# Optimization experiments

Hardware: AMD Instinct MI355X
Metric: run time of the kernel (lower is better)

Reference implementation:

```python
import jax, jax.numpy as jnp
import numpy as np
from jax import lax

# mamba-130m-style config
B, L = 2, 1024          # batch, seq_len
D = 768                 # hidden_size
E = 1536                # intermediate (expand=2)
N = 16                  # ssm state size
R = 48                  # time_step_rank = ceil(D/16)
K = 4                   # conv kernel
NL = 4                  # num layers
NC = 5                  # num classes
EPS = 1e-5


def setup_inputs() -> dict:
    key = jax.random.key(0)
    ks = jax.random.split(key, 10)
    s = 0.02
    return {
        "x": jax.random.normal(ks[0], (B, L, 12), dtype=jnp.float32),
        "proj_w": jax.random.normal(ks[1], (D, 12)) * s,
        "proj_b": jnp.zeros((D,), jnp.float32),
        "norm_w": jnp.ones((NL, D), jnp.float32),
        "in_w": jax.random.normal(ks[2], (NL, 2 * E, D)) * s,
        "conv_w": jax.random.normal(ks[3], (NL, E, K)) * s,
        "conv_b": jnp.zeros((NL, E), jnp.float32),
        "xproj_w": jax.random.normal(ks[4], (NL, R + 2 * N, E)) * s,
        "dt_w": jax.random.normal(ks[5], (NL, E, R)) * s,
        "dt_b": jnp.full((NL, E), -4.0, jnp.float32),  # softplus(-4) ~ small dt
        "A_log": jnp.tile(jnp.log(jnp.arange(1, N + 1, dtype=jnp.float32))[None, None, :], (NL, E, 1)),
        "D_param": jnp.ones((NL, E), jnp.float32),
        "out_w": jax.random.normal(ks[6], (NL, D, E)) * s,
        "fnorm_w": jnp.ones((D,), jnp.float32),
        "cls_w": jax.random.normal(ks[7], (NC, D)) * s,
        "cls_b": jnp.zeros((NC,), jnp.float32),
    }


def _rmsnorm(x, w):
    var = jnp.mean(x * x, axis=-1, keepdims=True)
    return x * lax.rsqrt(var + EPS) * w


def _causal_conv(u, w, b):
    # u: [B,L,E], w: [E,K] depthwise causal conv, left-pad K-1
    up = jnp.pad(u, ((0, 0), (K - 1, 0), (0, 0)))
    y = b
    for k in range(K):
        y = y + w[:, k] * up[:, k:k + L, :]
    return y


def _selective_scan(u, dt, A, Bm, Cm, Dp):
    # u, dt: [B,L,E]; Bm, Cm: [B,L,N]; A: [E,N]; Dp: [E]
    def step(h, inp):
        u_t, dt_t, B_t, C_t = inp  # [B,E],[B,E],[B,N],[B,N]
        dA = jnp.exp(dt_t[:, :, None] * A)                      # [B,E,N]
        h = h * dA + dt_t[:, :, None] * B_t[:, None, :] * u_t[:, :, None]
        y = jnp.einsum('ben,bn->be', h, C_t)
        return h, y

    h0 = jnp.zeros((u.shape[0], E, N), u.dtype)
    _, ys = lax.scan(step, h0,
                     (u.transpose(1, 0, 2), dt.transpose(1, 0, 2),
                      Bm.transpose(1, 0, 2), Cm.transpose(1, 0, 2)))
    return ys.transpose(1, 0, 2) + u * Dp


def reference(x, proj_w, proj_b, norm_w, in_w, conv_w, conv_b, xproj_w,
              dt_w, dt_b, A_log, D_param, out_w, fnorm_w, cls_w, cls_b):
    h = x @ proj_w.T + proj_b                                     # [B,L,D]
    for i in range(NL):
        res = h
        hn = _rmsnorm(h, norm_w[i])
        proj = hn @ in_w[i].T                                     # [B,L,2E]
        u, gate = proj[..., :E], proj[..., E:]
        u = jax.nn.silu(_causal_conv(u, conv_w[i], conv_b[i]))    # [B,L,E]
        xdbc = u @ xproj_w[i].T                                   # [B,L,R+2N]
        dt_r = xdbc[..., :R]
        Bm = xdbc[..., R:R + N]
        Cm = xdbc[..., R + N:]
        dt = jax.nn.softplus(dt_r @ dt_w[i].T + dt_b[i])          # [B,L,E]
        A = -jnp.exp(A_log[i])                                    # [E,N]
        y = _selective_scan(u, dt, A, Bm, Cm, D_param[i])
        y = y * jax.nn.silu(gate)
        h = res + y @ out_w[i].T
    h = _rmsnorm(h, fnorm_w)
    pooled = jnp.mean(h, axis=1)                                  # AdaptiveAvgPool1d(1)
    return pooled @ cls_w.T + cls_b                               # [B,NC]
```

## Files before the change

kernel.cpp:

```cpp
#include <hip/hip_runtime.h>

constexpr int B_  = 2;
constexpr int L_  = 1024;
constexpr int D_  = 768;
constexpr int E_  = 1536;
constexpr int N_  = 16;
constexpr int R_  = 48;
constexpr int NL_ = 4;
constexpr int NC_ = 5;
constexpr int M_  = B_ * L_;
constexpr int E2_ = 2 * E_;
constexpr int XD_ = R_ + 2 * N_;
constexpr float EPS_ = 1e-5f;

constexpr int NCH_ = 16;
constexpr int CL_  = L_ / NCH_;
constexpr int TS_  = 32;
constexpr int KS_  = 8;

typedef __attribute__((ext_vector_type(8))) short bf16x8;
typedef __attribute__((ext_vector_type(4))) float f32x4;
typedef const __attribute__((address_space(1))) void* gas_t;
typedef __attribute__((address_space(3))) void* las_t;

__device__ __forceinline__ float sigm(float x) { return 1.0f / (1.0f + __expf(-x)); }
__device__ __forceinline__ float softplusf(float x) { return x > 20.0f ? x : log1pf(__expf(x)); }
__device__ __forceinline__ ushort f2b(float f) {
  union { float f; unsigned u; } v; v.f = f;
  unsigned r = (v.u + 0x7fffu + ((v.u >> 16) & 1u)) >> 16;
  return (ushort)r;
}
__device__ __forceinline__ float b2f(ushort u) {
  union { unsigned u; float f; } v; v.u = ((unsigned)u) << 16;
  return v.f;
}
__device__ __forceinline__ float b2f_lo(unsigned p) {
  union { unsigned u; float f; } v; v.u = p << 16;
  return v.f;
}
__device__ __forceinline__ float b2f_hi(unsigned p) {
  union { unsigned u; float f; } v; v.u = p & 0xffff0000u;
  return v.f;
}

template <int CTRL>
__device__ __forceinline__ float dpp_add(float x) {
  int yi = __builtin_amdgcn_update_dpp(0, __builtin_bit_cast(int, x), CTRL, 0xf, 0xf, false);
  return x + __builtin_bit_cast(float, yi);
}
__device__ __forceinline__ float row_sum16(float x) {
  x = dpp_add<0x121>(x);
  x = dpp_add<0x122>(x);
  x = dpp_add<0x124>(x);
  x = dpp_add<0x128>(x);
  return x;
}

__device__ __forceinline__ float block_sum(float v, float* sm) {
  #pragma unroll
  for (int o = 32; o > 0; o >>= 1) v += __shfl_xor(v, o);
  if ((threadIdx.x & 63) == 0) sm[threadIdx.x >> 6] = v;
  __syncthreads();
  return sm[0] + sm[1] + sm[2] + sm[3];
}

constexpr int WS1_ = NL_ * E2_ * D_;
constexpr int WS2_ = NL_ * D_ * E_;
constexpr int WS3_ = NL_ * XD_ * E_;
constexpr int WS4_ = NL_ * E_ * 64;
__global__ __launch_bounds__(256) void k_wprep(const float* __restrict__ in_w, const float* __restrict__ out_w,
                                               const float* __restrict__ xw, const float* __restrict__ dw,
                                               ushort* __restrict__ in_wb, ushort* __restrict__ out_wb,
                                               ushort* __restrict__ xwb, ushort* __restrict__ dtwb) {
  int i = (blockIdx.x * 256 + threadIdx.x) * 4;
  if (i < WS1_) {
    float4 v = *(const float4*)(in_w + i);
    *(ushort4*)(in_wb + i) = make_ushort4(f2b(v.x), f2b(v.y), f2b(v.z), f2b(v.w));
  } else if (i < WS1_ + WS2_) {
    int j = i - WS1_;
    float4 v = *(const float4*)(out_w + j);
    *(ushort4*)(out_wb + j) = make_ushort4(f2b(v.x), f2b(v.y), f2b(v.z), f2b(v.w));
  } else if (i < WS1_ + WS2_ + WS3_) {
    int j = i - WS1_ - WS2_;
    float4 v = *(const float4*)(xw + j);
    *(ushort4*)(xwb + j) = make_ushort4(f2b(v.x), f2b(v.y), f2b(v.z), f2b(v.w));
  } else if (i < WS1_ + WS2_ + WS3_ + WS4_) {
    int j = i - WS1_ - WS2_ - WS3_;
    int k = j & 63, e = j >> 6;
    ushort4 o;
    o.x = (k + 0 < R_) ? f2b(dw[e * R_ + k + 0]) : (ushort)0;
    o.y = (k + 1 < R_) ? f2b(dw[e * R_ + k + 1]) : (ushort)0;
    o.z = (k + 2 < R_) ? f2b(dw[e * R_ + k + 2]) : (ushort)0;
    o.w = (k + 3 < R_) ? f2b(dw[e * R_ + k + 3]) : (ushort)0;
    *(ushort4*)(dtwb + j) = o;
  }
}

__global__ __launch_bounds__(256) void k_proj(const float* __restrict__ x, const float* __restrict__ pw,
                                              const float* __restrict__ pb, float* __restrict__ h) {
  __shared__ float xs[12];
  int m = blockIdx.y;
  int d = blockIdx.x * 256 + threadIdx.x;
  if (threadIdx.x < 12) xs[threadIdx.x] = x[m * 12 + threadIdx.x];
  __syncthreads();
  float acc = pb[d];
  #pragma unroll
  for (int j = 0; j < 12; j++) acc = fmaf(xs[j], pw[d * 12 + j], acc);
  h[(size_t)m * D_ + d] = acc;
}

__global__ __launch_bounds__(256) void k_rmsnorm_bf(const float* __restrict__ h, const float* __restrict__ w,
                                                    ushort* __restrict__ hn) {
  __shared__ float sm[4];
  int m = blockIdx.x, tid = threadIdx.x;
  const float* row = h + (size_t)m * D_;
  float v0 = row[tid], v1 = row[tid + 256], v2 = row[tid + 512];
  float s = block_sum(v0 * v0 + v1 * v1 + v2 * v2, sm);
  float sc = rsqrtf(s * (1.0f / D_) + EPS_);
  ushort* o = hn + (size_t)m * D_;
  o[tid]       = f2b(v0 * sc * w[tid]);
  o[tid + 256] = f2b(v1 * sc * w[tid + 256]);
  o[tid + 512] = f2b(v2 * sc * w[tid + 512]);
}

template <int BM, int BN, int MODE>
__global__ __launch_bounds__(256) void k_gemm_bf(const ushort* __restrict__ A, const ushort* __restrict__ Bw,
                                                 void* __restrict__ Cv, const float* __restrict__ res,
                                                 int Kd, int Nd) {
  constexpr int AM = BM / 32, BNF = BN / 32;
  __shared__ ushort sA[BM * 32];
  __shared__ ushort sB[BN * 32];
  const int tid = threadIdx.x;
  const int wave = tid >> 6, lane = tid & 63;
  const int q = lane >> 4, r = lane & 15;
  const int wm = wave >> 1, wn = wave & 1;
  const int m0 = blockIdx.y * BM, n0 = blockIdx.x * BN;
  f32x4 acc[AM][BNF] = {};

  for (int k0 = 0; k0 < Kd; k0 += 32) {
    #pragma unroll
    for (int j = 0; j < BM / 64; j++) {
      int i = j * 256 + tid;
      const ushort* gp = A + (size_t)(m0 + (i >> 2)) * Kd + k0 + ((i & 3) << 3);
      __builtin_amdgcn_global_load_lds((gas_t)gp, (las_t)(sA + ((j * 256 + wave * 64) << 3)), 16, 0, 0);
    }
    #pragma unroll
    for (int j = 0; j < BN / 64; j++) {
      int i = j * 256 + tid;
      const ushort* gp = Bw + (size_t)(n0 + (i >> 2)) * Kd + k0 + ((i & 3) << 3);
      __builtin_amdgcn_global_load_lds((gas_t)gp, (las_t)(sB + ((j * 256 + wave * 64) << 3)), 16, 0, 0);
    }
    __syncthreads();
    bf16x8 af[AM], bfv[BNF];
    #pragma unroll
    for (int mi = 0; mi < AM; mi++)
      af[mi] = *(const bf16x8*)&sA[(wm * (BM / 2) + mi * 16 + r) * 32 + q * 8];
    #pragma unroll
    for (int nj = 0; nj < BNF; nj++)
      bfv[nj] = *(const bf16x8*)&sB[(wn * (BN / 2) + nj * 16 + r) * 32 + q * 8];
    #pragma unroll
    for (int mi = 0; mi < AM; mi++)
      #pragma unroll
      for (int nj = 0; nj < BNF; nj++)
        acc[mi][nj] = __builtin_amdgcn_mfma_f32_16x16x32_bf16(af[mi], bfv[nj], acc[mi][nj], 0, 0, 0);
    __syncthreads();
  }
  #pragma unroll
  for (int mi = 0; mi < AM; mi++) {
    #pragma unroll
    for (int nj = 0; nj < BNF; nj++) {
      int col = n0 + wn * (BN / 2) + nj * 16 + r;
      #pragma unroll
      for (int rg = 0; rg < 4; rg++) {
        int row = m0 + wm * (BM / 2) + mi * 16 + q * 4 + rg;
        size_t off = (size_t)row * Nd + col;
        float v = acc[mi][nj][rg];
        if (MODE == 3) {
          ((ushort*)Cv)[off] = f2b(v);
        } else {
          if (MODE == 1) v += res[off];
          if (MODE == 2) v = softplusf(v + res[col]);
          ((float*)Cv)[off] = v;
        }
      }
    }
  }
}

__global__ __launch_bounds__(256) void k_gemm_x(const ushort* __restrict__ A, const ushort* __restrict__ Bw,
                                                float* __restrict__ part) {
  __shared__ ushort sA[64 * 32];
  __shared__ ushort sB[80 * 32];
  const int tid = threadIdx.x;
  const int wave = tid >> 6, lane = tid & 63;
  const int q = lane >> 4, r = lane & 15;
  const int m0 = blockIdx.x * 64;
  const int kbeg = blockIdx.y * (E_ / KS_), kend = kbeg + E_ / KS_;
  f32x4 acc[5] = {};

  for (int k0 = kbeg; k0 < kend; k0 += 32) {
    {
      const ushort* gp = A + (size_t)(m0 + wave * 16 + (lane >> 2)) * E_ + k0 + ((lane & 3) << 3);
      __builtin_amdgcn_global_load_lds((gas_t)gp, (las_t)(sA + (wave << 9)), 16, 0, 0);
    }
    #pragma unroll
    for (int j = wave; j < 5; j += 4) {
      const ushort* gp = Bw + (size_t)(j * 16 + (lane >> 2)) * E_ + k0 + ((lane & 3) << 3);
      __builtin_amdgcn_global_load_lds((gas_t)gp, (las_t)(sB + (j << 9)), 16, 0, 0);
    }
    __syncthreads();
    bf16x8 af = *(const bf16x8*)&sA[(wave * 16 + r) * 32 + q * 8];
    #pragma unroll
    for (int nj = 0; nj < 5; nj++) {
      bf16x8 bfv = *(const bf16x8*)&sB[(nj * 16 + r) * 32 + q * 8];
      acc[nj] = __builtin_amdgcn_mfma_f32_16x16x32_bf16(af, bfv, acc[nj], 0, 0, 0);
    }
    __syncthreads();
  }
  float* pp = part + (size_t)blockIdx.y * M_ * XD_;
  #pragma unroll
  for (int nj = 0; nj < 5; nj++) {
    int col = nj * 16 + r;
    #pragma unroll
    for (int rg = 0; rg < 4; rg++) {
      int row = m0 + wave * 16 + q * 4 + rg;
      pp[(size_t)row * XD_ + col] = acc[nj][rg];
    }
  }
}

__global__ __launch_bounds__(256) void k_xfin(const float* __restrict__ part, float* __restrict__ xdbc,
                                              ushort* __restrict__ xb) {
  int i = blockIdx.x * 256 + threadIdx.x;
  int m = i / XD_, col = i - m * XD_;
  float s = 0.0f;
  #pragma unroll
  for (int ks = 0; ks < KS_; ks++) s += part[(size_t)ks * M_ * XD_ + i];
  xdbc[i] = s;
  if (col < R_) xb[(size_t)m * 64 + col] = f2b(s);
  else if (col < 64) xb[(size_t)m * 64 + col] = 0;
}

__global__ __launch_bounds__(384) void k_conv2(const ushort* __restrict__ proj, const float* __restrict__ cw,
                                               const float* __restrict__ cb, ushort* __restrict__ ub16,
                                               ushort* __restrict__ gb16) {
  int m = blockIdx.x;
  int b = m >> 10, t = m & (L_ - 1);
  int e4 = threadIdx.x * 4;
  float wv[4][4];
  #pragma unroll
  for (int j = 0; j < 4; j++) {
    float4 w = *(const float4*)(cw + (e4 + j) * 4);
    wv[j][0] = w.x; wv[j][1] = w.y; wv[j][2] = w.z; wv[j][3] = w.w;
  }
  float4 bb = *(const float4*)(cb + e4);
  float acc[4] = {bb.x, bb.y, bb.z, bb.w};
  #pragma unroll
  for (int k = 0; k < 4; k++) {
    int tt = t + k - 3;
    if (tt >= 0) {
      uint2 p = *(const uint2*)(proj + (size_t)(b * L_ + tt) * E2_ + e4);
      acc[0] = fmaf(wv[0][k], b2f_lo(p.x), acc[0]);
      acc[1] = fmaf(wv[1][k], b2f_hi(p.x), acc[1]);
      acc[2] = fmaf(wv[2][k], b2f_lo(p.y), acc[2]);
      acc[3] = fmaf(wv[3][k], b2f_hi(p.y), acc[3]);
    }
  }
  uint2 uo;
  {
    float u0 = acc[0] * sigm(acc[0]), u1 = acc[1] * sigm(acc[1]);
    float u2 = acc[2] * sigm(acc[2]), u3 = acc[3] * sigm(acc[3]);
    uo.x = (unsigned)f2b(u0) | ((unsigned)f2b(u1) << 16);
    uo.y = (unsigned)f2b(u2) | ((unsigned)f2b(u3) << 16);
  }
  *(uint2*)(ub16 + (size_t)m * E_ + e4) = uo;
  uint2 g = *(const uint2*)(proj + (size_t)m * E2_ + E_ + e4);
  float g0 = b2f_lo(g.x), g1 = b2f_hi(g.x), g2 = b2f_lo(g.y), g3 = b2f_hi(g.y);
  g0 *= sigm(g0); g1 *= sigm(g1); g2 *= sigm(g2); g3 *= sigm(g3);
  uint2 go;
  go.x = (unsigned)f2b(g0) | ((unsigned)f2b(g1) << 16);
  go.y = (unsigned)f2b(g2) | ((unsigned)f2b(g3) << 16);
  *(uint2*)(gb16 + (size_t)m * E_ + e4) = go;
}

__global__ __launch_bounds__(256) void k_scanA(const ushort* __restrict__ u, const float* __restrict__ dtb,
                                               const float* __restrict__ xdbc, const float* __restrict__ A_log,
                                               float* __restrict__ Pst, float* __restrict__ Sst) {
  __shared__ float2 s_dtu[2][TS_][16];
  __shared__ float  s_b [2][TS_][16];
  const int tid = threadIdx.x;
  const int e0 = blockIdx.x << 4;
  const int b  = blockIdx.y;
  const int c  = blockIdx.z;
  const int n  = tid & 15, el = tid >> 4;
  const int e  = e0 + el;
  const float A = -__expf(A_log[e * N_ + n]);
  const int se = tid & 15, st = tid >> 4;

  float r_dt[2], r_b[2];
  ushort r_u[2];
  auto issue = [&](int s) {
    int t0 = c * CL_ + s * TS_;
    #pragma unroll
    for (int j = 0; j < 2; j++) {
      size_t m = (size_t)(b * L_ + t0 + j * 16 + st);
      r_dt[j] = dtb[m * E_ + e0 + se];
      r_u[j]  = u[m * E_ + e0 + se];
    }
    #pragma unroll
    for (int j = 0; j < 2; j++) {
      int idx = j * 256 + tid;
      r_b[j] = xdbc[(size_t)(b * L_ + t0 + (idx >> 4)) * XD_ + R_ + (idx & 15)];
    }
  };
  auto commit = [&](int pb) {
    #pragma unroll
    for (int j = 0; j < 2; j++) {
      int t = j * 16 + st;
      s_dtu[pb][t][se] = make_float2(r_dt[j], r_dt[j] * b2f(r_u[j]));
    }
    #pragma unroll
    for (int j = 0; j < 2; j++) {
      int idx = j * 256 + tid;
      s_b[pb][idx >> 4][idx & 15] = r_b[j];
    }
  };

  issue(0);
  commit(0);
  float hs = 0.0f, pp = 1.0f;
  constexpr int NS = CL_ / TS_;
  for (int s = 0; s < NS; s++) {
    __syncthreads();
    if (s + 1 < NS) issue(s + 1);
    const int pb = s & 1;
    #pragma unroll
    for (int t = 0; t < TS_; t++) {
      float2 dtu = s_dtu[pb][t][el];
      float bv   = s_b[pb][t][n];
      float dA = __expf(dtu.x * A);
      hs = fmaf(hs, dA, dtu.y * bv);
      pp *= dA;
    }
    if (s + 1 < NS) commit((s + 1) & 1);
  }
  size_t o = (((size_t)(b * NCH_ + c) * E_) + e) * N_ + n;
  Pst[o] = pp;
  Sst[o] = hs;
}

__global__ __launch_bounds__(256) void k_scanC(const ushort* __restrict__ u, const float* __restrict__ dtb,
                                               const float* __restrict__ xdbc, const ushort* __restrict__ gb,
                                               const float* __restrict__ A_log, const float* __restrict__ Dp,
                                               const float* __restrict__ Pst, const float* __restrict__ Sst,
                                               ushort* __restrict__ y) {
  __shared__ float2 s_dtu[2][TS_][16];
  __shared__ float2 s_bc [2][TS_][16];
  __shared__ float2 s_og [2][TS_][16];
  const int tid = threadIdx.x;
  const int e0 = blockIdx.x << 4;
  const int b  = blockIdx.y;
  const int c  = blockIdx.z;
  const int n  = tid & 15, el = tid >> 4;
  const int e  = e0 + el;
  const float A = -__expf(A_log[e * N_ + n]);
  const int se = tid & 15, st = tid >> 4;
  const float Dv = Dp[e0 + se];

  float r_dt[2], r_bc[4];
  ushort r_u[2], r_g[2];
  auto issue = [&](int s) {
    int t0 = c * CL_ + s * TS_;
    #pragma unroll
    for (int j = 0; j < 2; j++) {
      size_t m = (size_t)(b * L_ + t0 + j * 16 + st);
      r_dt[j] = dtb[m * E_ + e0 + se];
      r_u[j]  = u[m * E_ + e0 + se];
      r_g[j]  = gb[m * E_ + e0 + se];
    }
    #pragma unroll
    for (int j = 0; j < 4; j++) {
      int idx = j * 256 + tid;
      r_bc[j] = xdbc[(size_t)(b * L_ + t0 + (idx >> 5)) * XD_ + R_ + (idx & 31)];
    }
  };
  auto commit = [&](int pb) {
    #pragma unroll
    for (int j = 0; j < 2; j++) {
      int t = j * 16 + st;
      float uf = b2f(r_u[j]);
      s_dtu[pb][t][se] = make_float2(r_dt[j], r_dt[j] * uf);
      s_og[pb][t][se] = make_float2(uf * Dv, b2f(r_g[j]));
    }
    #pragma unroll
    for (int j = 0; j < 4; j++) {
      int idx = j * 256 + tid;
      int t = idx >> 5, col = idx & 31;
      ((float*)&s_bc[pb][t][0])[((col & 15) << 1) + (col >> 4)] = r_bc[j];
    }
  };

  issue(0);
  float hs = 0.0f;
  for (int cc = 0; cc < c; cc++) {
    size_t o = (((size_t)(b * NCH_ + cc) * E_) + e) * N_ + n;
    hs = fmaf(Pst[o], hs, Sst[o]);
  }
  commit(0);
  constexpr int NS = CL_ / TS_;
  for (int s = 0; s < NS; s++) {
    __syncthreads();
    if (s + 1 < NS) issue(s + 1);
    const int pb = s & 1;
    const int mbase = b * L_ + c * CL_ + s * TS_;
    #pragma unroll
    for (int t = 0; t < TS_; t++) {
      float2 dtu = s_dtu[pb][t][el];
      float2 bc  = s_bc[pb][t][n];
      float dA = __expf(dtu.x * A);
      hs = fmaf(hs, dA, dtu.y * bc.x);
      float p = row_sum16(hs * bc.y);
      if (n == 0) {
        float2 og = s_og[pb][t][el];
        y[(size_t)(mbase + t) * E_ + e] = f2b((p + og.x) * og.y);
      }
    }
    if (s + 1 < NS) commit((s + 1) & 1);
  }
}

__global__ __launch_bounds__(256) void k_rowscale(const float* __restrict__ h, float* __restrict__ rs) {
  __shared__ float sm[4];
  int m = blockIdx.x, tid = threadIdx.x;
  const float* row = h + (size_t)m * D_;
  float v0 = row[tid], v1 = row[tid + 256], v2 = row[tid + 512];
  float s = block_sum(v0 * v0 + v1 * v1 + v2 * v2, sm);
  if (tid == 0) rs[m] = rsqrtf(s * (1.0f / D_) + EPS_);
}

__global__ __launch_bounds__(256) void k_pool(const float* __restrict__ h, const float* __restrict__ rs,
                                              const float* __restrict__ fw, float* __restrict__ pooled) {
  int d = blockIdx.x * 256 + threadIdx.x;
  int t0 = blockIdx.y * 128;
  int b = blockIdx.z;
  float acc = 0.0f;
  for (int t = t0; t < t0 + 128; t++) {
    int m = b * L_ + t;
    acc = fmaf(h[(size_t)m * D_ + d], rs[m], acc);
  }
  atomicAdd(&pooled[b * D_ + d], acc * fw[d] * (1.0f / L_));
}

__global__ __launch_bounds__(256) void k_logits(const float* __restrict__ pooled, const float* __restrict__ cw,
                                                const float* __restrict__ cb, float* __restrict__ out) {
  int wv = threadIdx.x >> 6, ln = threadIdx.x & 63;
  for (int p = wv; p < B_ * NC_; p += 4) {
    int b = p / NC_, c = p % NC_;
    float s = 0.0f;
    for (int d = ln; d < D_; d += 64) s = fmaf(pooled[b * D_ + d], cw[c * D_ + d], s);
    #pragma unroll
    for (int o = 32; o > 0; o >>= 1) s += __shfl_xor(s, o);
    if (ln == 0) out[p] = s + cb[c];
  }
}

extern "C" void kernel_launch(void* const* d_in, const int* in_sizes, int n_in,
                              void* d_out, int out_size, void* d_ws, size_t ws_size,
                              hipStream_t stream) {
  const float* x       = (const float*)d_in[0];
  const float* proj_w  = (const float*)d_in[1];
  const float* proj_b  = (const float*)d_in[2];
  const float* norm_w  = (const float*)d_in[3];
  const float* in_w    = (const float*)d_in[4];
  const float* conv_w  = (const float*)d_in[5];
  const float* conv_b  = (const float*)d_in[6];
  const float* xproj_w = (const float*)d_in[7];
  const float* dt_w    = (const float*)d_in[8];
  const float* dt_b    = (const float*)d_in[9];
  const float* A_log   = (const float*)d_in[10];
  const float* D_param = (const float*)d_in[11];
  const float* out_w   = (const float*)d_in[12];
  const float* fnorm_w = (const float*)d_in[13];
  const float* cls_w   = (const float*)d_in[14];
  const float* cls_b   = (const float*)d_in[15];
  float* out = (float*)d_out;

  float* h      = (float*)d_ws;
  float* xdbc   = h + (size_t)M_ * D_;
  float* dtbuf  = xdbc + (size_t)M_ * XD_;
  float* rsb    = dtbuf + (size_t)M_ * E_;
  float* pooled = rsb + M_;
  float* Pst    = pooled + B_ * D_;
  float* Sst    = Pst + (size_t)B_ * NCH_ * E_ * N_;
  float* xpart  = Sst + (size_t)B_ * NCH_ * E_ * N_;
  ushort* proj_bf = (ushort*)(xpart + (size_t)KS_ * M_ * XD_);
  ushort* hn_bf   = proj_bf + (size_t)M_ * E2_;
  ushort* y_bf    = hn_bf + (size_t)M_ * D_;
  ushort* ub_bf   = y_bf + (size_t)M_ * E_;
  ushort* g_bf    = ub_bf + (size_t)M_ * E_;
  ushort* xdbc_bf = g_bf + (size_t)M_ * E_;
  ushort* xwb     = xdbc_bf + (size_t)M_ * 64;
  ushort* dtwb    = xwb + (size_t)NL_ * XD_ * E_;
  ushort* in_wb   = dtwb + (size_t)NL_ * E_ * 64;
  ushort* out_wb  = in_wb + (size_t)NL_ * E2_ * D_;

  constexpr int WTOT = WS1_ + WS2_ + WS3_ + WS4_;
  k_wprep<<<(WTOT / 4 + 255) / 256, 256, 0, stream>>>(in_w, out_w, xproj_w, dt_w,
                                                      in_wb, out_wb, xwb, dtwb);

  k_proj<<<dim3(D_ / 256, M_), 256, 0, stream>>>(x, proj_w, proj_b, h);

  for (int i = 0; i < NL_; i++) {
    k_rmsnorm_bf<<<M_, 256, 0, stream>>>(h, norm_w + i * D_, hn_bf);
    k_gemm_bf<64, 128, 3><<<dim3(E2_ / 128, M_ / 64), 256, 0, stream>>>(
        hn_bf, in_wb + (size_t)i * E2_ * D_, proj_bf, nullptr, D_, E2_);
    k_conv2<<<M_, 384, 0, stream>>>(proj_bf, conv_w + i * E_ * 4, conv_b + i * E_, ub_bf, g_bf);
    k_gemm_x<<<dim3(M_ / 64, KS_), 256, 0, stream>>>(ub_bf, xwb + (size_t)i * XD_ * E_, xpart);
    k_xfin<<<M_ * XD_ / 256, 256, 0, stream>>>(xpart, xdbc, xdbc_bf);
    k_gemm_bf<64, 64, 2><<<dim3(E_ / 64, M_ / 64), 256, 0, stream>>>(
        xdbc_bf, dtwb + (size_t)i * E_ * 64, dtbuf, dt_b + i * E_, 64, E_);
    k_scanA<<<dim3(E_ / 16, B_, NCH_), 256, 0, stream>>>(ub_bf, dtbuf, xdbc,
                                                         A_log + (size_t)i * E_ * N_, Pst, Sst);
    k_scanC<<<dim3(E_ / 16, B_, NCH_), 256, 0, stream>>>(ub_bf, dtbuf, xdbc, g_bf,
                                                         A_log + (size_t)i * E_ * N_, D_param + i * E_,
                                                         Pst, Sst, y_bf);
    k_gemm_bf<64, 64, 1><<<dim3(D_ / 64, M_ / 64), 256, 0, stream>>>(
        y_bf, out_wb + (size_t)i * D_ * E_, h, h, E_, D_);
  }

  k_rowscale<<<M_, 256, 0, stream>>>(h, rsb);
  hipMemsetAsync(pooled, 0, (size_t)B_ * D_ * sizeof(float), stream);
  k_pool<<<dim3(D_ / 256, L_ / 128, B_), 256, 0, stream>>>(h, rsb, fnorm_w, pooled);
  k_logits<<<1, 256, 0, stream>>>(pooled, cls_w, cls_b, out);
}
```

Baseline: 692.2 us.

## Fuse causal conv into x-proj GEMM, gate SiLU into in-proj epilogue, bf16 dt

The standalone conv kernel is removed. The depthwise causal conv plus SiLU is now computed inside the x-projection GEMM, which stages a whole K-slice of u and weights in LDS and still writes u to global for the scan. The gate SiLU moves into the in-projection GEMM epilogue, and the scan reads the gate straight from the projection buffer. The dt projection now stores softplus output as bf16 instead of fp32, which halves the dt traffic read by both scan kernels but lowers dt precision. The fused GEMM uses a large LDS footprint and recomputes conv loads per block, which may reduce occupancy.

```diff
diff --git a/kernel.cpp b/kernel.cpp
--- a/kernel.cpp
+++ b/kernel.cpp
@@ -17,6 +17,8 @@
 constexpr int CL_  = L_ / NCH_;
 constexpr int TS_  = 32;
 constexpr int KS_  = 8;
+constexpr int XSL_ = E_ / KS_;
+constexpr int USTR_ = 200;
 
 typedef __attribute__((ext_vector_type(8))) short bf16x8;
 typedef __attribute__((ext_vector_type(4))) float f32x4;
@@ -175,11 +177,13 @@
         int row = m0 + wm * (BM / 2) + mi * 16 + q * 4 + rg;
         size_t off = (size_t)row * Nd + col;
         float v = acc[mi][nj][rg];
-        if (MODE == 3) {
+        if (MODE == 4) {
+          if (col >= (Nd >> 1)) v = v * sigm(v);
           ((ushort*)Cv)[off] = f2b(v);
+        } else if (MODE == 6) {
+          ((ushort*)Cv)[off] = f2b(softplusf(v + res[col]));
         } else {
           if (MODE == 1) v += res[off];
-          if (MODE == 2) v = softplusf(v + res[col]);
           ((float*)Cv)[off] = v;
         }
       }
@@ -187,35 +191,66 @@
   }
 }
 
-__global__ __launch_bounds__(256) void k_gemm_x(const ushort* __restrict__ A, const ushort* __restrict__ Bw,
-                                                float* __restrict__ part) {
-  __shared__ ushort sA[64 * 32];
-  __shared__ ushort sB[80 * 32];
+__global__ __launch_bounds__(256) void k_gemm_xc(const ushort* __restrict__ proj, const float* __restrict__ cw,
+                                                 const float* __restrict__ cb, const ushort* __restrict__ Bw,
+                                                 ushort* __restrict__ ub16, float* __restrict__ part) {
+  __shared__ ushort sU[64 * USTR_];
+  __shared__ ushort sB[80 * USTR_];
   const int tid = threadIdx.x;
   const int wave = tid >> 6, lane = tid & 63;
   const int q = lane >> 4, r = lane & 15;
   const int m0 = blockIdx.x * 64;
-  const int kbeg = blockIdx.y * (E_ / KS_), kend = kbeg + E_ / KS_;
+  const int kbeg = blockIdx.y * XSL_;
+
+  for (int i = tid; i < 80 * (XSL_ / 8); i += 256) {
+    int row = i / (XSL_ / 8), seg = i % (XSL_ / 8);
+    bf16x8 v = *(const bf16x8*)(Bw + (size_t)row * E_ + kbeg + seg * 8);
+    *(bf16x8*)&sB[row * USTR_ + seg * 8] = v;
+  }
+
+  for (int i = tid; i < 64 * (XSL_ / 4); i += 256) {
+    int row = i / (XSL_ / 4), e4i = i % (XSL_ / 4);
+    int e = kbeg + e4i * 4;
+    int m = m0 + row;
+    int t = m & (L_ - 1);
+    float4 w0 = *(const float4*)(cw + (e + 0) * 4);
+    float4 w1 = *(const float4*)(cw + (e + 1) * 4);
+    float4 w2 = *(const float4*)(cw + (e + 2) * 4);
+    float4 w3 = *(const float4*)(cw + (e + 3) * 4);
+    float wv[4][4] = {{w0.x, w0.y, w0.z, w0.w}, {w1.x, w1.y, w1.z, w1.w},
+                      {w2.x, w2.y, w2.z, w2.w}, {w3.x, w3.y, w3.z, w3.w}};
+    float4 bb = *(const float4*)(cb + e);
+    float acc[4] = {bb.x, bb.y, bb.z, bb.w};
+    #pragma unroll
+    for (int k = 0; k < 4; k++) {
+      int tt = t + k - 3;
+      if (tt >= 0) {
+        uint2 p = *(const uint2*)(proj + (size_t)(m + k - 3) * E2_ + e);
+        acc[0] = fmaf(wv[0][k], b2f_lo(p.x), acc[0]);
+        acc[1] = fmaf(wv[1][k], b2f_hi(p.x), acc[1]);
+        acc[2] = fmaf(wv[2][k], b2f_lo(p.y), acc[2]);
+        acc[3] = fmaf(wv[3][k], b2f_hi(p.y), acc[3]);
+      }
+    }
+    float u0 = acc[0] * sigm(acc[0]), u1 = acc[1] * sigm(acc[1]);
+    float u2 = acc[2] * sigm(acc[2]), u3 = acc[3] * sigm(acc[3]);
+    uint2 uo;
+    uo.x = (unsigned)f2b(u0) | ((unsigned)f2b(u1) << 16);
+    uo.y = (unsigned)f2b(u2) | ((unsigned)f2b(u3) << 16);
+    *(uint2*)(ub16 + (size_t)m * E_ + e) = uo;
+    *(uint2*)&sU[row * USTR_ + e4i * 4] = uo;
+  }
+  __syncthreads();
+
   f32x4 acc[5] = {};
-
-  for (int k0 = kbeg; k0 < kend; k0 += 32) {
-    {
-      const ushort* gp = A + (size_t)(m0 + wave * 16 + (lane >> 2)) * E_ + k0 + ((lane & 3) << 3);
-      __builtin_amdgcn_global_load_lds((gas_t)gp, (las_t)(sA + (wave << 9)), 16, 0, 0);
-    }
-    #pragma unroll
-    for (int j = wave; j < 5; j += 4) {
-      const ushort* gp = Bw + (size_t)(j * 16 + (lane >> 2)) * E_ + k0 + ((lane & 3) << 3);
-      __builtin_amdgcn_global_load_lds((gas_t)gp, (las_t)(sB + (j << 9)), 16, 0, 0);
-    }
-    __syncthreads();
-    bf16x8 af = *(const bf16x8*)&sA[(wave * 16 + r) * 32 + q * 8];
+  #pragma unroll
+  for (int k0 = 0; k0 < XSL_ / 32; k0++) {
+    bf16x8 af = *(const bf16x8*)&sU[(wave * 16 + r) * USTR_ + k0 * 32 + q * 8];
     #pragma unroll
     for (int nj = 0; nj < 5; nj++) {
-      bf16x8 bfv = *(const bf16x8*)&sB[(nj * 16 + r) * 32 + q * 8];
+      bf16x8 bfv = *(const bf16x8*)&sB[(nj * 16 + r) * USTR_ + k0 * 32 + q * 8];
       acc[nj] = __builtin_amdgcn_mfma_f32_16x16x32_bf16(af, bfv, acc[nj], 0, 0, 0);
     }
-    __syncthreads();
   }
   float* pp = part + (size_t)blockIdx.y * M_ * XD_;
   #pragma unroll
@@ -241,49 +276,7 @@
   else if (col < 64) xb[(size_t)m * 64 + col] = 0;
 }
 
-__global__ __launch_bounds__(384) void k_conv2(const ushort* __restrict__ proj, const float* __restrict__ cw,
-                                               const float* __restrict__ cb, ushort* __restrict__ ub16,
-                                               ushort* __restrict__ gb16) {
-  int m = blockIdx.x;
-  int b = m >> 10, t = m & (L_ - 1);
-  int e4 = threadIdx.x * 4;
-  float wv[4][4];
-  #pragma unroll
-  for (int j = 0; j < 4; j++) {
-    float4 w = *(const float4*)(cw + (e4 + j) * 4);
-    wv[j][0] = w.x; wv[j][1] = w.y; wv[j][2] = w.z; wv[j][3] = w.w;
-  }
-  float4 bb = *(const float4*)(cb + e4);
-  float acc[4] = {bb.x, bb.y, bb.z, bb.w};
-  #pragma unroll
-  for (int k = 0; k < 4; k++) {
-    int tt = t + k - 3;
-    if (tt >= 0) {
-      uint2 p = *(const uint2*)(proj + (size_t)(b * L_ + tt) * E2_ + e4);
-      acc[0] = fmaf(wv[0][k], b2f_lo(p.x), acc[0]);
-      acc[1] = fmaf(wv[1][k], b2f_hi(p.x), acc[1]);
-      acc[2] = fmaf(wv[2][k], b2f_lo(p.y), acc[2]);
-      acc[3] = fmaf(wv[3][k], b2f_hi(p.y), acc[3]);
-    }
-  }
-  uint2 uo;
-  {
-    float u0 = acc[0] * sigm(acc[0]), u1 = acc[1] * sigm(acc[1]);
-    float u2 = acc[2] * sigm(acc[2]), u3 = acc[3] * sigm(acc[3]);
-    uo.x = (unsigned)f2b(u0) | ((unsigned)f2b(u1) << 16);
-    uo.y = (unsigned)f2b(u2) | ((unsigned)f2b(u3) << 16);
-  }
-  *(uint2*)(ub16 + (size_t)m * E_ + e4) = uo;
-  uint2 g = *(const uint2*)(proj + (size_t)m * E2_ + E_ + e4);
-  float g0 = b2f_lo(g.x), g1 = b2f_hi(g.x), g2 = b2f_lo(g.y), g3 = b2f_hi(g.y);
-  g0 *= sigm(g0); g1 *= sigm(g1); g2 *= sigm(g2); g3 *= sigm(g3);
-  uint2 go;
-  go.x = (unsigned)f2b(g0) | ((unsigned)f2b(g1) << 16);
-  go.y = (unsigned)f2b(g2) | ((unsigned)f2b(g3) << 16);
-  *(uint2*)(gb16 + (size_t)m * E_ + e4) = go;
-}
-
-__global__ __launch_bounds__(256) void k_scanA(const ushort* __restrict__ u, const float* __restrict__ dtb,
+__global__ __launch_bounds__(256) void k_scanA(const ushort* __restrict__ u, const ushort* __restrict__ dtb,
                                                const float* __restrict__ xdbc, const float* __restrict__ A_log,
                                                float* __restrict__ Pst, float* __restrict__ Sst) {
   __shared__ float2 s_dtu[2][TS_][16];
@@ -297,8 +290,8 @@
   const float A = -__expf(A_log[e * N_ + n]);
   const int se = tid & 15, st = tid >> 4;
 
-  float r_dt[2], r_b[2];
-  ushort r_u[2];
+  float r_b[2];
+  ushort r_dt[2], r_u[2];
   auto issue = [&](int s) {
     int t0 = c * CL_ + s * TS_;
     #pragma unroll
@@ -317,7 +310,8 @@
     #pragma unroll
     for (int j = 0; j < 2; j++) {
       int t = j * 16 + st;
-      s_dtu[pb][t][se] = make_float2(r_dt[j], r_dt[j] * b2f(r_u[j]));
+      float dtv = b2f(r_dt[j]);
+      s_dtu[pb][t][se] = make_float2(dtv, dtv * b2f(r_u[j]));
     }
     #pragma unroll
     for (int j = 0; j < 2; j++) {
@@ -349,8 +343,8 @@
   Sst[o] = hs;
 }
 
-__global__ __launch_bounds__(256) void k_scanC(const ushort* __restrict__ u, const float* __restrict__ dtb,
-                                               const float* __restrict__ xdbc, const ushort* __restrict__ gb,
+__global__ __launch_bounds__(256) void k_scanC(const ushort* __restrict__ u, const ushort* __restrict__ dtb,
+                                               const float* __restrict__ xdbc, const ushort* __restrict__ proj,
                                                const float* __restrict__ A_log, const float* __restrict__ Dp,
                                                const float* __restrict__ Pst, const float* __restrict__ Sst,
                                                ushort* __restrict__ y) {
@@ -367,8 +361,8 @@
   const int se = tid & 15, st = tid >> 4;
   const float Dv = Dp[e0 + se];
 
-  float r_dt[2], r_bc[4];
-  ushort r_u[2], r_g[2];
+  float r_bc[4];
+  ushort r_dt[2], r_u[2], r_g[2];
   auto issue = [&](int s) {
     int t0 = c * CL_ + s * TS_;
     #pragma unroll
@@ -376,7 +370,7 @@
       size_t m = (size_t)(b * L_ + t0 + j * 16 + st);
       r_dt[j] = dtb[m * E_ + e0 + se];
       r_u[j]  = u[m * E_ + e0 + se];
-      r_g[j]  = gb[m * E_ + e0 + se];
+      r_g[j]  = proj[m * E2_ + E_ + e0 + se];
     }
     #pragma unroll
     for (int j = 0; j < 4; j++) {
@@ -388,8 +382,9 @@
     #pragma unroll
     for (int j = 0; j < 2; j++) {
       int t = j * 16 + st;
+      float dtv = b2f(r_dt[j]);
       float uf = b2f(r_u[j]);
-      s_dtu[pb][t][se] = make_float2(r_dt[j], r_dt[j] * uf);
+      s_dtu[pb][t][se] = make_float2(dtv, dtv * uf);
       s_og[pb][t][se] = make_float2(uf * Dv, b2f(r_g[j]));
     }
     #pragma unroll
@@ -487,8 +482,7 @@
 
   float* h      = (float*)d_ws;
   float* xdbc   = h + (size_t)M_ * D_;
-  float* dtbuf  = xdbc + (size_t)M_ * XD_;
-  float* rsb    = dtbuf + (size_t)M_ * E_;
+  float* rsb    = xdbc + (size_t)M_ * XD_;
   float* pooled = rsb + M_;
   float* Pst    = pooled + B_ * D_;
   float* Sst    = Pst + (size_t)B_ * NCH_ * E_ * N_;
@@ -497,8 +491,8 @@
   ushort* hn_bf   = proj_bf + (size_t)M_ * E2_;
   ushort* y_bf    = hn_bf + (size_t)M_ * D_;
   ushort* ub_bf   = y_bf + (size_t)M_ * E_;
-  ushort* g_bf    = ub_bf + (size_t)M_ * E_;
-  ushort* xdbc_bf = g_bf + (size_t)M_ * E_;
+  ushort* dt_bf   = ub_bf + (size_t)M_ * E_;
+  ushort* xdbc_bf = dt_bf + (size_t)M_ * E_;
   ushort* xwb     = xdbc_bf + (size_t)M_ * 64;
   ushort* dtwb    = xwb + (size_t)NL_ * XD_ * E_;
   ushort* in_wb   = dtwb + (size_t)NL_ * E_ * 64;
@@ -512,16 +506,16 @@
 
   for (int i = 0; i < NL_; i++) {
     k_rmsnorm_bf<<<M_, 256, 0, stream>>>(h, norm_w + i * D_, hn_bf);
-    k_gemm_bf<64, 128, 3><<<dim3(E2_ / 128, M_ / 64), 256, 0, stream>>>(
+    k_gemm_bf<64, 128, 4><<<dim3(E2_ / 128, M_ / 64), 256, 0, stream>>>(
         hn_bf, in_wb + (size_t)i * E2_ * D_, proj_bf, nullptr, D_, E2_);
-    k_conv2<<<M_, 384, 0, stream>>>(proj_bf, conv_w + i * E_ * 4, conv_b + i * E_, ub_bf, g_bf);
-    k_gemm_x<<<dim3(M_ / 64, KS_), 256, 0, stream>>>(ub_bf, xwb + (size_t)i * XD_ * E_, xpart);
+    k_gemm_xc<<<dim3(M_ / 64, KS_), 256, 0, stream>>>(proj_bf, conv_w + i * E_ * 4, conv_b + i * E_,
+                                                      xwb + (size_t)i * XD_ * E_, ub_bf, xpart);
     k_xfin<<<M_ * XD_ / 256, 256, 0, stream>>>(xpart, xdbc, xdbc_bf);
-    k_gemm_bf<64, 64, 2><<<dim3(E_ / 64, M_ / 64), 256, 0, stream>>>(
-        xdbc_bf, dtwb + (size_t)i * E_ * 64, dtbuf, dt_b + i * E_, 64, E_);
-    k_scanA<<<dim3(E_ / 16, B_, NCH_), 256, 0, stream>>>(ub_bf, dtbuf, xdbc,
+    k_gemm_bf<64, 64, 6><<<dim3(E_ / 64, M_ / 64), 256, 0, stream>>>(
+        xdbc_bf, dtwb + (size_t)i * E_ * 64, dt_bf, dt_b + i * E_, 64, E_);
+    k_scanA<<<dim3(E_ / 16, B_, NCH_), 256, 0, stream>>>(ub_bf, dt_bf, xdbc,
                                                          A_log + (size_t)i * E_ * N_, Pst, Sst);
-    k_scanC<<<dim3(E_ / 16, B_, NCH_), 256, 0, stream>>>(ub_bf, dtbuf, xdbc, g_bf,
+    k_scanC<<<dim3(E_ / 16, B_, NCH_), 256, 0, stream>>>(ub_bf, dt_bf, xdbc, proj_bf,
                                                          A_log + (size_t)i * E_ * N_, D_param + i * E_,
                                                          Pst, Sst, y_bf);
     k_gemm_bf<64, 64, 1><<<dim3(D_ / 64, M_ / 64), 256, 0, stream>>>(
```

Result: slower. 715.8 us (+3.4%).

## Load whole scan chunk up front, batch y stores, drop memset and pool atomics

Applied to the files above, without the earlier changes.

The scan kernels now load the full 64-step chunk into shared memory in one go instead of double-buffering 32-step tiles. k_scanC prefetches all previous-chunk prefix states with unrolled loads, stages y in shared memory, and writes it with coalesced vector stores instead of scattered 2-byte stores. The pooling step writes per-chunk partial sums that the logits kernel reduces, which removes the memset and the atomics. These changes trade more registers and shared memory per block, with an occupancy hint of 6, for fewer syncs and better memory access patterns.

```diff
diff --git a/kernel.cpp b/kernel.cpp
--- a/kernel.cpp
+++ b/kernel.cpp
@@ -15,8 +15,8 @@
 
 constexpr int NCH_ = 16;
 constexpr int CL_  = L_ / NCH_;
-constexpr int TS_  = 32;
 constexpr int KS_  = 8;
+constexpr int PC_  = 8;
 
 typedef __attribute__((ext_vector_type(8))) short bf16x8;
 typedef __attribute__((ext_vector_type(4))) float f32x4;
@@ -283,11 +283,11 @@
   *(uint2*)(gb16 + (size_t)m * E_ + e4) = go;
 }
 
-__global__ __launch_bounds__(256) void k_scanA(const ushort* __restrict__ u, const float* __restrict__ dtb,
-                                               const float* __restrict__ xdbc, const float* __restrict__ A_log,
-                                               float* __restrict__ Pst, float* __restrict__ Sst) {
-  __shared__ float2 s_dtu[2][TS_][16];
-  __shared__ float  s_b [2][TS_][16];
+__global__ __launch_bounds__(256, 6) void k_scanA(const ushort* __restrict__ u, const float* __restrict__ dtb,
+                                                  const float* __restrict__ xdbc, const float* __restrict__ A_log,
+                                                  float* __restrict__ Pst, float* __restrict__ Sst) {
+  __shared__ float2 s_dtu[CL_][16];
+  __shared__ float  s_b [CL_][16];
   const int tid = threadIdx.x;
   const int e0 = blockIdx.x << 4;
   const int b  = blockIdx.y;
@@ -295,68 +295,49 @@
   const int n  = tid & 15, el = tid >> 4;
   const int e  = e0 + el;
   const float A = -__expf(A_log[e * N_ + n]);
-  const int se = tid & 15, st = tid >> 4;
-
-  float r_dt[2], r_b[2];
-  ushort r_u[2];
-  auto issue = [&](int s) {
-    int t0 = c * CL_ + s * TS_;
-    #pragma unroll
-    for (int j = 0; j < 2; j++) {
-      size_t m = (size_t)(b * L_ + t0 + j * 16 + st);
-      r_dt[j] = dtb[m * E_ + e0 + se];
-      r_u[j]  = u[m * E_ + e0 + se];
-    }
-    #pragma unroll
-    for (int j = 0; j < 2; j++) {
-      int idx = j * 256 + tid;
-      r_b[j] = xdbc[(size_t)(b * L_ + t0 + (idx >> 4)) * XD_ + R_ + (idx & 15)];
-    }
-  };
-  auto commit = [&](int pb) {
-    #pragma unroll
-    for (int j = 0; j < 2; j++) {
-      int t = j * 16 + st;
-      s_dtu[pb][t][se] = make_float2(r_dt[j], r_dt[j] * b2f(r_u[j]));
-    }
-    #pragma unroll
-    for (int j = 0; j < 2; j++) {
-      int idx = j * 256 + tid;
-      s_b[pb][idx >> 4][idx & 15] = r_b[j];
-    }
-  };
-
-  issue(0);
-  commit(0);
+  const int t0 = c * CL_;
+
+  float r_dt[4], r_b[4];
+  ushort r_u[4];
+  #pragma unroll
+  for (int j = 0; j < 4; j++) {
+    size_t m = (size_t)(b * L_ + t0 + j * 16 + el);
+    r_dt[j] = dtb[m * E_ + e0 + n];
+    r_u[j]  = u[m * E_ + e0 + n];
+    int idx = j * 256 + tid;
+    r_b[j] = xdbc[(size_t)(b * L_ + t0 + (idx >> 4)) * XD_ + R_ + (idx & 15)];
+  }
+  #pragma unroll
+  for (int j = 0; j < 4; j++) {
+    int t = j * 16 + el;
+    s_dtu[t][n] = make_float2(r_dt[j], r_dt[j] * b2f(r_u[j]));
+    int idx = j * 256 + tid;
+    s_b[idx >> 4][idx & 15] = r_b[j];
+  }
+  __syncthreads();
+
   float hs = 0.0f, pp = 1.0f;
-  constexpr int NS = CL_ / TS_;
-  for (int s = 0; s < NS; s++) {
-    __syncthreads();
-    if (s + 1 < NS) issue(s + 1);
-    const int pb = s & 1;
-    #pragma unroll
-    for (int t = 0; t < TS_; t++) {
-      float2 dtu = s_dtu[pb][t][el];
-      float bv   = s_b[pb][t][n];
-      float dA = __expf(dtu.x * A);
-      hs = fmaf(hs, dA, dtu.y * bv);
-      pp *= dA;
-    }
-    if (s + 1 < NS) commit((s + 1) & 1);
+  #pragma unroll 8
+  for (int t = 0; t < CL_; t++) {
+    float2 dtu = s_dtu[t][el];
+    float dA = __expf(dtu.x * A);
+    hs = fmaf(hs, dA, dtu.y * s_b[t][n]);
+    pp *= dA;
   }
   size_t o = (((size_t)(b * NCH_ + c) * E_) + e) * N_ + n;
   Pst[o] = pp;
   Sst[o] = hs;
 }
 
-__global__ __launch_bounds__(256) void k_scanC(const ushort* __restrict__ u, const float* __restrict__ dtb,
-                                               const float* __restrict__ xdbc, const ushort* __restrict__ gb,
-                                               const float* __restrict__ A_log, const float* __restrict__ Dp,
-                                               const float* __restrict__ Pst, const float* __restrict__ Sst,
-                                               ushort* __restrict__ y) {
-  __shared__ float2 s_dtu[2][TS_][16];
-  __shared__ float2 s_bc [2][TS_][16];
-  __shared__ float2 s_og [2][TS_][16];
+__global__ __launch_bounds__(256, 6) void k_scanC(const ushort* __restrict__ u, const float* __restrict__ dtb,
+                                                  const float* __restrict__ xdbc, const ushort* __restrict__ gb,
+                                                  const float* __restrict__ A_log, const float* __restrict__ Dp,
+                                                  const float* __restrict__ Pst, const float* __restrict__ Sst,
+                                                  ushort* __restrict__ y) {
+  __shared__ float2 s_dtu[CL_][16];
+  __shared__ float2 s_bc [CL_][16];
+  __shared__ float2 s_og [CL_][16];
+  __shared__ ushort s_y [CL_][16];
   const int tid = threadIdx.x;
   const int e0 = blockIdx.x << 4;
   const int b  = blockIdx.y;
@@ -364,68 +345,74 @@
   const int n  = tid & 15, el = tid >> 4;
   const int e  = e0 + el;
   const float A = -__expf(A_log[e * N_ + n]);
-  const int se = tid & 15, st = tid >> 4;
-  const float Dv = Dp[e0 + se];
-
-  float r_dt[2], r_bc[4];
-  ushort r_u[2], r_g[2];
-  auto issue = [&](int s) {
-    int t0 = c * CL_ + s * TS_;
-    #pragma unroll
-    for (int j = 0; j < 2; j++) {
-      size_t m = (size_t)(b * L_ + t0 + j * 16 + st);
-      r_dt[j] = dtb[m * E_ + e0 + se];
-      r_u[j]  = u[m * E_ + e0 + se];
-      r_g[j]  = gb[m * E_ + e0 + se];
-    }
-    #pragma unroll
-    for (int j = 0; j < 4; j++) {
-      int idx = j * 256 + tid;
-      r_bc[j] = xdbc[(size_t)(b * L_ + t0 + (idx >> 5)) * XD_ + R_ + (idx & 31)];
-    }
-  };
-  auto commit = [&](int pb) {
-    #pragma unroll
-    for (int j = 0; j < 2; j++) {
-      int t = j * 16 + st;
-      float uf = b2f(r_u[j]);
-      s_dtu[pb][t][se] = make_float2(r_dt[j], r_dt[j] * uf);
-      s_og[pb][t][se] = make_float2(uf * Dv, b2f(r_g[j]));
-    }
-    #pragma unroll
-    for (int j = 0; j < 4; j++) {
-      int idx = j * 256 + tid;
-      int t = idx >> 5, col = idx & 31;
-      ((float*)&s_bc[pb][t][0])[((col & 15) << 1) + (col >> 4)] = r_bc[j];
-    }
-  };
-
-  issue(0);
+  const float Dv = Dp[e0 + n];
+  const int t0 = c * CL_;
+
+  float r_dt[4], r_bc[8];
+  ushort r_u[4], r_g[4];
+  #pragma unroll
+  for (int j = 0; j < 4; j++) {
+    size_t m = (size_t)(b * L_ + t0 + j * 16 + el);
+    r_dt[j] = dtb[m * E_ + e0 + n];
+    r_u[j]  = u[m * E_ + e0 + n];
+    r_g[j]  = gb[m * E_ + e0 + n];
+  }
+  #pragma unroll
+  for (int j = 0; j < 8; j++) {
+    int idx = j * 256 + tid;
+    r_bc[j] = xdbc[(size_t)(b * L_ + t0 + (idx >> 5)) * XD_ + R_ + (idx & 31)];
+  }
+
   float hs = 0.0f;
-  for (int cc = 0; cc < c; cc++) {
-    size_t o = (((size_t)(b * NCH_ + cc) * E_) + e) * N_ + n;
-    hs = fmaf(Pst[o], hs, Sst[o]);
-  }
-  commit(0);
-  constexpr int NS = CL_ / TS_;
-  for (int s = 0; s < NS; s++) {
-    __syncthreads();
-    if (s + 1 < NS) issue(s + 1);
-    const int pb = s & 1;
-    const int mbase = b * L_ + c * CL_ + s * TS_;
-    #pragma unroll
-    for (int t = 0; t < TS_; t++) {
-      float2 dtu = s_dtu[pb][t][el];
-      float2 bc  = s_bc[pb][t][n];
-      float dA = __expf(dtu.x * A);
-      hs = fmaf(hs, dA, dtu.y * bc.x);
-      float p = row_sum16(hs * bc.y);
-      if (n == 0) {
-        float2 og = s_og[pb][t][el];
-        y[(size_t)(mbase + t) * E_ + e] = f2b((p + og.x) * og.y);
-      }
-    }
-    if (s + 1 < NS) commit((s + 1) & 1);
+  if (c > 0) {
+    float pv[NCH_ - 1], sv[NCH_ - 1];
+    #pragma unroll
+    for (int cc = 0; cc < NCH_ - 1; cc++) {
+      int ci = cc < c ? cc : c - 1;
+      size_t o = (((size_t)(b * NCH_ + ci) * E_) + e) * N_ + n;
+      pv[cc] = Pst[o];
+      sv[cc] = Sst[o];
+    }
+    #pragma unroll
+    for (int cc = 0; cc < NCH_ - 1; cc++) {
+      bool v = cc < c;
+      hs = fmaf(v ? pv[cc] : 1.0f, hs, v ? sv[cc] : 0.0f);
+    }
+  }
+
+  #pragma unroll
+  for (int j = 0; j < 4; j++) {
+    int t = j * 16 + el;
+    float uf = b2f(r_u[j]);
+    s_dtu[t][n] = make_float2(r_dt[j], r_dt[j] * uf);
+    s_og[t][n] = make_float2(uf * Dv, b2f(r_g[j]));
+  }
+  #pragma unroll
+  for (int j = 0; j < 8; j++) {
+    int idx = j * 256 + tid;
+    int t = idx >> 5, col = idx & 31;
+    ((float*)&s_bc[t][0])[((col & 15) << 1) + (col >> 4)] = r_bc[j];
+  }
+  __syncthreads();
+
+  #pragma unroll 8
+  for (int t = 0; t < CL_; t++) {
+    float2 dtu = s_dtu[t][el];
+    float2 bc  = s_bc[t][n];
+    float dA = __expf(dtu.x * A);
+    hs = fmaf(hs, dA, dtu.y * bc.x);
+    float p = row_sum16(hs * bc.y);
+    if (n == 0) {
+      float2 og = s_og[t][el];
+      s_y[t][el] = f2b((p + og.x) * og.y);
+    }
+  }
+  __syncthreads();
+
+  {
+    int row = tid >> 2, seg = tid & 3;
+    uint2 v = *(const uint2*)&s_y[row][seg * 4];
+    *(uint2*)(y + (size_t)(b * L_ + t0 + row) * E_ + e0 + seg * 4) = v;
   }
 }
 
@@ -439,28 +426,35 @@
 }
 
 __global__ __launch_bounds__(256) void k_pool(const float* __restrict__ h, const float* __restrict__ rs,
-                                              const float* __restrict__ fw, float* __restrict__ pooled) {
+                                              float* __restrict__ pooledP) {
   int d = blockIdx.x * 256 + threadIdx.x;
-  int t0 = blockIdx.y * 128;
+  int pc = blockIdx.y;
   int b = blockIdx.z;
+  int t0 = pc * (L_ / PC_);
   float acc = 0.0f;
-  for (int t = t0; t < t0 + 128; t++) {
+  for (int t = t0; t < t0 + L_ / PC_; t++) {
     int m = b * L_ + t;
     acc = fmaf(h[(size_t)m * D_ + d], rs[m], acc);
   }
-  atomicAdd(&pooled[b * D_ + d], acc * fw[d] * (1.0f / L_));
-}
-
-__global__ __launch_bounds__(256) void k_logits(const float* __restrict__ pooled, const float* __restrict__ cw,
-                                                const float* __restrict__ cb, float* __restrict__ out) {
+  pooledP[((size_t)pc * B_ + b) * D_ + d] = acc;
+}
+
+__global__ __launch_bounds__(256) void k_logits(const float* __restrict__ pooledP, const float* __restrict__ fw,
+                                                const float* __restrict__ cw, const float* __restrict__ cb,
+                                                float* __restrict__ out) {
   int wv = threadIdx.x >> 6, ln = threadIdx.x & 63;
   for (int p = wv; p < B_ * NC_; p += 4) {
     int b = p / NC_, c = p % NC_;
     float s = 0.0f;
-    for (int d = ln; d < D_; d += 64) s = fmaf(pooled[b * D_ + d], cw[c * D_ + d], s);
+    for (int d = ln; d < D_; d += 64) {
+      float pd = 0.0f;
+      #pragma unroll
+      for (int pc = 0; pc < PC_; pc++) pd += pooledP[((size_t)pc * B_ + b) * D_ + d];
+      s = fmaf(pd * fw[d], cw[c * D_ + d], s);
+    }
     #pragma unroll
     for (int o = 32; o > 0; o >>= 1) s += __shfl_xor(s, o);
-    if (ln == 0) out[p] = s + cb[c];
+    if (ln == 0) out[p] = s * (1.0f / L_) + cb[c];
   }
 }
 
@@ -489,8 +483,8 @@
   float* xdbc   = h + (size_t)M_ * D_;
   float* dtbuf  = xdbc + (size_t)M_ * XD_;
   float* rsb    = dtbuf + (size_t)M_ * E_;
-  float* pooled = rsb + M_;
-  float* Pst    = pooled + B_ * D_;
+  float* pooledP = rsb + M_;
+  float* Pst    = pooledP + (size_t)PC_ * B_ * D_;
   float* Sst    = Pst + (size_t)B_ * NCH_ * E_ * N_;
   float* xpart  = Sst + (size_t)B_ * NCH_ * E_ * N_;
   ushort* proj_bf = (ushort*)(xpart + (size_t)KS_ * M_ * XD_);
@@ -529,7 +523,6 @@
   }
 
   k_rowscale<<<M_, 256, 0, stream>>>(h, rsb);
-  hipMemsetAsync(pooled, 0, (size_t)B_ * D_ * sizeof(float), stream);
-  k_pool<<<dim3(D_ / 256, L_ / 128, B_), 256, 0, stream>>>(h, rsb, fnorm_w, pooled);
-  k_logits<<<1, 256, 0, stream>>>(pooled, cls_w, cls_b, out);
-}
+  k_pool<<<dim3(D_ / 256, PC_, B_), 256, 0, stream>>>(h, rsb, pooledP);
+  k_logits<<<1, 256, 0, stream>>>(pooledP, fnorm_w, cls_w, cls_b, out);
+}
```

New measurement: 732.5 us. +5.8%, slower.
